# Kernel tuning notes

Hardware: AMD Instinct MI355X
Metric: run time of the kernel (lower is better)

Reference implementation:

```python
import jax, jax.numpy as jnp
import numpy as np

B, C, H, W = 4, 256, 64, 64
CH = C // 2  # inner channels


def setup_inputs() -> dict:
    key = jax.random.key(0)
    ks = jax.random.split(key, 9)
    s_in = 1.0 / np.sqrt(C)
    s_w = 1.0 / np.sqrt(CH)
    return {
        "x": jax.random.normal(ks[0], (B, C, H, W), dtype=jnp.float32),
        "theta_w": jax.random.normal(ks[1], (CH, C), dtype=jnp.float32) * s_in,
        "theta_b": jax.random.normal(ks[2], (CH,), dtype=jnp.float32) * s_in,
        "phi_w": jax.random.normal(ks[3], (CH, C), dtype=jnp.float32) * s_in,
        "phi_b": jax.random.normal(ks[4], (CH,), dtype=jnp.float32) * s_in,
        "g_w": jax.random.normal(ks[5], (CH, C), dtype=jnp.float32) * s_in,
        "g_b": jax.random.normal(ks[6], (CH,), dtype=jnp.float32) * s_in,
        "W_w": jax.random.normal(ks[7], (C, CH), dtype=jnp.float32) * s_w,
        "W_b": jax.random.normal(ks[8], (C,), dtype=jnp.float32) * s_w,
    }


def _proj(x_flat, w, b):
    # 1x1 conv == channel matmul; x_flat: [B, C, N] -> [B, O, N]
    return jnp.einsum("oc,bcn->bon", w, x_flat) + b[None, :, None]


def reference(x, theta_w, theta_b, phi_w, phi_b, g_w, g_b, W_w, W_b):
    b, c, h, w = x.shape
    n = h * w
    xf = x.reshape(b, c, n)
    theta = _proj(xf, theta_w, theta_b)  # [B, CH, N]
    phi = _proj(xf, phi_w, phi_b)        # [B, CH, N]
    g = _proj(xf, g_w, g_b)              # [B, CH, N]
    # scores[b,i,j] = theta[:, :, i] . phi[:, :, j]; softmax over j
    attn = jax.nn.softmax(jnp.einsum("bci,bcj->bij", theta, phi), axis=-1)
    # torch: bmm(g_x, attn) -> out[b,c,i] = sum_j g[b,c,j] * attn[b,j,i]
    out = jnp.einsum("bcj,bji->bci", g, attn)  # [B, CH, N]
    out = jnp.einsum("oc,bcn->bon", W_w, out) + W_b[None, :, None]
    return out.reshape(b, c, h, w) + x
```

## Files before the change

### kernel.cpp

```cpp
#include <hip/hip_runtime.h>
#include <hip/hip_bf16.h>
#include <math.h>

#define BB    4
#define CC    256
#define CHN   128
#define NN    4096

typedef short short8 __attribute__((ext_vector_type(8)));
typedef float f32x4  __attribute__((ext_vector_type(4)));
typedef unsigned short u16;
typedef u16  us4 __attribute__((ext_vector_type(4)));

#define MFMA16(a, b, c) __builtin_amdgcn_mfma_f32_16x16x32_bf16((a), (b), (c), 0, 0, 0)
#define LOG2E 1.4426950408889634f

#if __has_builtin(__builtin_amdgcn_exp2f)
#define EXP2F(x) __builtin_amdgcn_exp2f(x)
#else
#define EXP2F(x) exp2f(x)
#endif
#if __has_builtin(__builtin_amdgcn_logf)
#define LOG2F(x) __builtin_amdgcn_logf(x)
#else
#define LOG2F(x) log2f(x)
#endif

static __device__ __forceinline__ u16 f2bf(float f) {
    union { float f; unsigned u; } v; v.f = f;
    unsigned r = v.u + 0x7FFFu + ((v.u >> 16) & 1u);
    return (u16)(r >> 16);
}
static __device__ __forceinline__ unsigned pkbf(float a, float b) {
    __hip_bfloat162 h = __float22bfloat162_rn(make_float2(a, b));
    return *reinterpret_cast<unsigned*>(&h);
}
static __device__ __forceinline__ int sw128(int row, int u) {
    return row * 128 + ((u ^ (row & 7)) << 3);
}

__global__ __launch_bounds__(256) void k_cvtw(
    const float* __restrict__ tw, const float* __restrict__ pw,
    const float* __restrict__ gw, const float* __restrict__ Ww,
    u16* __restrict__ wall)
{
    int idx = (blockIdx.x * 256 + threadIdx.x) * 4;
    const float* s = (idx < 32768) ? tw
                   : (idx < 65536) ? pw
                   : (idx < 98304) ? gw : Ww;
    float sc = (idx < 32768) ? LOG2E : 1.0f;
    float4 v = *(const float4*)(s + (idx & 32767));
    us4 r = { f2bf(v.x * sc), f2bf(v.y * sc), f2bf(v.z * sc), f2bf(v.w * sc) };
    *(us4*)(wall + idx) = r;
}

__global__ __launch_bounds__(512) void k_proj(
    const float* __restrict__ x, const u16* __restrict__ wall,
    const float* __restrict__ tb, const float* __restrict__ pb,
    const float* __restrict__ gbias,
    u16* __restrict__ tht, u16* __restrict__ pht, u16* __restrict__ gg)
{
    __shared__ u16 xs[64 * 264];
    __shared__ u16 gbuf[128 * 68];
    const int tid = threadIdx.x;
    const int n0  = blockIdx.x * 64;
    const int b   = blockIdx.y;
    const int ln  = tid & 15, q = (tid >> 4) & 3, wid = tid >> 6;
    const int ow  = wid & 1, nw = wid >> 1;

    for (int p = 0; p < 8; ++p) {
        int id = p * 512 + tid;
        int c = id >> 4, n4 = (id & 15) * 4;
        float4 xv = *(const float4*)(x + ((size_t)b * CC + c) * NN + n0 + n4);
        xs[(n4 + 0) * 264 + c] = f2bf(xv.x);
        xs[(n4 + 1) * 264 + c] = f2bf(xv.y);
        xs[(n4 + 2) * 264 + c] = f2bf(xv.z);
        xs[(n4 + 3) * 264 + c] = f2bf(xv.w);
    }
    __syncthreads();

    short8 bfr[8];
    #pragma unroll
    for (int ks = 0; ks < 8; ++ks)
        bfr[ks] = *(const short8*)(&xs[(nw * 16 + ln) * 264 + ks * 32 + q * 8]);

    for (int pr = 0; pr < 3; ++pr) {
        const u16* wsrc = wall + pr * 32768;
        f32x4 acc[4];
        #pragma unroll
        for (int oo = 0; oo < 4; ++oo) acc[oo] = (f32x4){0.f, 0.f, 0.f, 0.f};
        for (int ks = 0; ks < 8; ++ks) {
            short8 a[4];
            #pragma unroll
            for (int oo = 0; oo < 4; ++oo)
                a[oo] = *(const short8*)(wsrc + (size_t)(ow*64 + oo*16 + ln) * 256 + ks*32 + q*8);
            #pragma unroll
            for (int oo = 0; oo < 4; ++oo)
                acc[oo] = MFMA16(a[oo], bfr[ks], acc[oo]);
        }
        const float* bias = (pr == 0) ? tb : (pr == 1 ? pb : gbias);
        const float bsc = (pr == 0) ? LOG2E : 1.0f;
        if (pr < 2) {
            u16* dst = (pr == 0) ? tht : pht;
            const int n = n0 + nw * 16 + ln;
            #pragma unroll
            for (int oo = 0; oo < 4; ++oo) {
                int o = ow * 64 + oo * 16 + q * 4;
                float4 bv = *(const float4*)(bias + o);
                f32x4 v = acc[oo];
                uint2 r = { pkbf(v.x + bv.x * bsc, v.y + bv.y * bsc),
                            pkbf(v.z + bv.z * bsc, v.w + bv.w * bsc) };
                *(uint2*)(dst + ((size_t)b * NN + n) * CHN + o) = r;
            }
        } else {
            const int nl = nw * 16 + ln;
            #pragma unroll
            for (int oo = 0; oo < 4; ++oo) {
                int o = ow * 64 + oo * 16 + q * 4;
                float4 bv = *(const float4*)(bias + o);
                f32x4 v = acc[oo];
                gbuf[(o + 0) * 68 + nl] = f2bf(v.x + bv.x);
                gbuf[(o + 1) * 68 + nl] = f2bf(v.y + bv.y);
                gbuf[(o + 2) * 68 + nl] = f2bf(v.z + bv.z);
                gbuf[(o + 3) * 68 + nl] = f2bf(v.w + bv.w);
            }
            __syncthreads();
            for (int p = 0; p < 4; ++p) {
                int id = p * 512 + tid;
                int c = id >> 4, n4 = (id & 15) * 4;
                us4 r = *(const us4*)(&gbuf[c * 68 + n4]);
                *(us4*)(gg + ((size_t)b * CHN + c) * NN + n0 + n4) = r;
            }
        }
    }
}

__global__ __launch_bounds__(512) void k_rowsum(
    const u16* __restrict__ tht, const u16* __restrict__ pht,
    float* __restrict__ Z)
{
    __shared__ u16 th_s[128 * 128];
    __shared__ u16 ph_s[128 * 128];
    __shared__ float zs[128][2];
    const int tid = threadIdx.x;
    const int j0  = blockIdx.x * 128;
    const int ih  = blockIdx.y;
    const int b   = blockIdx.z;
    const int ln  = tid & 15, q = (tid >> 4) & 3, wid = tid >> 6;
    const int jw  = wid & 3, iw = wid >> 2;

    {
        const u16* src = tht + ((size_t)b * NN + j0) * CHN;
        for (int p = 0; p < 4; ++p) {
            int id = p * 512 + tid;
            int row = id >> 4, u = id & 15;
            short8 v = *(const short8*)(src + row * 128 + u * 8);
            *(short8*)(&th_s[sw128(row, u)]) = v;
        }
    }
    __syncthreads();
    short8 ar[2][4];
    #pragma unroll
    for (int jj = 0; jj < 2; ++jj)
        #pragma unroll
        for (int ks = 0; ks < 4; ++ks)
            ar[jj][ks] = *(const short8*)(&th_s[sw128(jw*32 + jj*16 + ln, ks*4 + q)]);

    float zp[2][4];
    #pragma unroll
    for (int jj = 0; jj < 2; ++jj)
        #pragma unroll
        for (int r = 0; r < 4; ++r) zp[jj][r] = 0.f;

    const u16* phb = pht + ((size_t)b * NN + ih * 2048) * CHN;
    for (int is = 0; is < 16; ++is) {
        __syncthreads();
        for (int p = 0; p < 4; ++p) {
            int id = p * 512 + tid;
            int row = id >> 4, u = id & 15;
            short8 v = *(const short8*)(phb + (size_t)(is * 128 + row) * CHN + u * 8);
            *(short8*)(&ph_s[sw128(row, u)]) = v;
        }
        __syncthreads();

        f32x4 s[2][4];
        #pragma unroll
        for (int jj = 0; jj < 2; ++jj)
            #pragma unroll
            for (int ii = 0; ii < 4; ++ii) s[jj][ii] = (f32x4){0.f, 0.f, 0.f, 0.f};
        for (int ks = 0; ks < 4; ++ks) {
            short8 bb[4];
            #pragma unroll
            for (int ii = 0; ii < 4; ++ii)
                bb[ii] = *(const short8*)(&ph_s[sw128(iw*64 + ii*16 + ln, ks*4 + q)]);
            #pragma unroll
            for (int jj = 0; jj < 2; ++jj)
                #pragma unroll
                for (int ii = 0; ii < 4; ++ii)
                    s[jj][ii] = MFMA16(ar[jj][ks], bb[ii], s[jj][ii]);
        }
        #pragma unroll
        for (int jj = 0; jj < 2; ++jj)
            #pragma unroll
            for (int ii = 0; ii < 4; ++ii) {
                f32x4 v = s[jj][ii];
                zp[jj][0] += EXP2F(v.x);
                zp[jj][1] += EXP2F(v.y);
                zp[jj][2] += EXP2F(v.z);
                zp[jj][3] += EXP2F(v.w);
            }
    }

    #pragma unroll
    for (int jj = 0; jj < 2; ++jj)
        #pragma unroll
        for (int r = 0; r < 4; ++r) {
            float v = zp[jj][r];
            v += __shfl_xor(v, 1);
            v += __shfl_xor(v, 2);
            v += __shfl_xor(v, 4);
            v += __shfl_xor(v, 8);
            if (ln == 0) zs[jw*32 + jj*16 + q*4 + r][iw] = v;
        }
    __syncthreads();
    if (tid < 128)
        atomicAdd(&Z[(size_t)b * NN + j0 + tid], zs[tid][0] + zs[tid][1]);
}

__global__ __launch_bounds__(512, 2) void k_attn(
    const u16* __restrict__ tht, const u16* __restrict__ pht,
    const u16* __restrict__ gg, const float* __restrict__ Z,
    u16* __restrict__ innerT)
{
    __shared__ u16 th_s[128 * 128];
    __shared__ u16 g_s [128 * 128];
    __shared__ u16 E_s [256 * 128];
    const int tid = threadIdx.x;
    const int i0  = blockIdx.x * 256;
    const int jq  = blockIdx.y;
    const int b   = blockIdx.z;
    const int ln  = tid & 15, q = (tid >> 4) & 3, wid = tid >> 6;
    const int h1  = wid & 1;
    const int h2  = wid >> 1;

    const u16*  thb = tht + (size_t)b * NN * CHN;
    const u16*  ggb = gg  + (size_t)b * CHN * NN;
    const float* Zb = Z   + (size_t)b * NN;

    {
        const u16* src = pht + ((size_t)b * NN + i0) * CHN;
        for (int p = 0; p < 8; ++p) {
            int id = p * 512 + tid;
            int row = id >> 4, u = id & 15;
            short8 v = *(const short8*)(src + row * 128 + u * 8);
            *(short8*)(&E_s[sw128(row, u)]) = v;
        }
    }
    __syncthreads();
    short8 phr[4][4];
    #pragma unroll
    for (int ii = 0; ii < 4; ++ii)
        #pragma unroll
        for (int ks = 0; ks < 4; ++ks)
            phr[ii][ks] = *(const short8*)(&E_s[sw128(h2*64 + ii*16 + ln, ks*4 + q)]);

    f32x4 pacc[4][4];
    #pragma unroll
    for (int cc = 0; cc < 4; ++cc)
        #pragma unroll
        for (int ii = 0; ii < 4; ++ii) pacc[cc][ii] = (f32x4){0.f, 0.f, 0.f, 0.f};

    for (int js = 0; js < 8; ++js) {
        const int j0 = jq * 1024 + js * 128;
        __syncthreads();
        for (int p = 0; p < 4; ++p) {
            int id = p * 512 + tid;
            int row = id >> 4, u = id & 15;
            short8 v = *(const short8*)(thb + (size_t)(j0 + row) * CHN + u * 8);
            *(short8*)(&th_s[sw128(row, u)]) = v;
        }
        for (int p = 0; p < 4; ++p) {
            int id = p * 512 + tid;
            int row = id >> 4, u = id & 15;
            short8 v = *(const short8*)(ggb + (size_t)row * NN + j0 + u * 8);
            *(short8*)(&g_s[sw128(row, u)]) = v;
        }
        __syncthreads();

        #pragma unroll
        for (int jj = 0; jj < 4; ++jj) {
            const int jl = h1*64 + jj*16 + q*4;
            float4 Zv = *(const float4*)(Zb + j0 + jl);
            f32x4 cinit = { -LOG2F(Zv.x), -LOG2F(Zv.y), -LOG2F(Zv.z), -LOG2F(Zv.w) };
            f32x4 s0 = cinit, s1 = cinit, s2 = cinit, s3 = cinit;
            #pragma unroll
            for (int ks = 0; ks < 4; ++ks) {
                short8 a = *(const short8*)(&th_s[sw128(h1*64 + jj*16 + ln, ks*4 + q)]);
                s0 = MFMA16(a, phr[0][ks], s0);
                s1 = MFMA16(a, phr[1][ks], s1);
                s2 = MFMA16(a, phr[2][ks], s2);
                s3 = MFMA16(a, phr[3][ks], s3);
            }
            const int u = jl >> 3, off = jl & 7;
            f32x4 sv[4] = { s0, s1, s2, s3 };
            #pragma unroll
            for (int ii = 0; ii < 4; ++ii) {
                int ri = h2*64 + ii*16 + ln;
                f32x4 v = sv[ii];
                uint2 e = { pkbf(EXP2F(v.x), EXP2F(v.y)),
                            pkbf(EXP2F(v.z), EXP2F(v.w)) };
                *(uint2*)(&E_s[ri*128 + ((u ^ (ri & 7)) << 3) + off]) = e;
            }
        }
        __syncthreads();

        #pragma unroll
        for (int ks = 0; ks < 4; ++ks) {
            short8 be[4];
            #pragma unroll
            for (int ii = 0; ii < 4; ++ii)
                be[ii] = *(const short8*)(&E_s[sw128(h2*64 + ii*16 + ln, ks*4 + q)]);
            #pragma unroll
            for (int cc = 0; cc < 4; ++cc) {
                short8 ag = *(const short8*)(&g_s[sw128(h1*64 + cc*16 + ln, ks*4 + q)]);
                pacc[cc][0] = MFMA16(ag, be[0], pacc[cc][0]);
                pacc[cc][1] = MFMA16(ag, be[1], pacc[cc][1]);
                pacc[cc][2] = MFMA16(ag, be[2], pacc[cc][2]);
                pacc[cc][3] = MFMA16(ag, be[3], pacc[cc][3]);
            }
        }
    }

    u16* dst = innerT + ((size_t)jq * BB + b) * (size_t)NN * CHN;
    #pragma unroll
    for (int cc = 0; cc < 4; ++cc)
        #pragma unroll
        for (int ii = 0; ii < 4; ++ii) {
            int i = i0 + h2*64 + ii*16 + ln;
            int c = h1*64 + cc*16 + q*4;
            f32x4 v = pacc[cc][ii];
            uint2 r = { pkbf(v.x, v.y), pkbf(v.z, v.w) };
            *(uint2*)(dst + (size_t)i * CHN + c) = r;
        }
}

__global__ __launch_bounds__(512) void k_final(
    const u16* __restrict__ innerT, const float* __restrict__ x,
    const u16* __restrict__ Wwbf, const float* __restrict__ Wb,
    float* __restrict__ out)
{
    const int tid = threadIdx.x;
    const int n0  = blockIdx.x * 64;
    const int b   = blockIdx.y;
    const int ln  = tid & 15, q = (tid >> 4) & 3, wid = tid >> 6;

    f32x4 acc[4][2];
    #pragma unroll
    for (int nn = 0; nn < 4; ++nn)
        #pragma unroll
        for (int oo = 0; oo < 2; ++oo) acc[nn][oo] = (f32x4){0.f, 0.f, 0.f, 0.f};

    for (int jq = 0; jq < 4; ++jq) {
        const u16* src = innerT + ((size_t)jq * BB + b) * (size_t)NN * CHN;
        for (int ks = 0; ks < 4; ++ks) {
            short8 a[4], bw[2];
            #pragma unroll
            for (int nn = 0; nn < 4; ++nn)
                a[nn] = *(const short8*)(src + (size_t)(n0 + nn*16 + ln) * CHN + ks*32 + q*8);
            #pragma unroll
            for (int oo = 0; oo < 2; ++oo)
                bw[oo] = *(const short8*)(Wwbf + (size_t)(wid*32 + oo*16 + ln) * CHN + ks*32 + q*8);
            #pragma unroll
            for (int nn = 0; nn < 4; ++nn)
                #pragma unroll
                for (int oo = 0; oo < 2; ++oo)
                    acc[nn][oo] = MFMA16(a[nn], bw[oo], acc[nn][oo]);
        }
    }
    #pragma unroll
    for (int nn = 0; nn < 4; ++nn)
        #pragma unroll
        for (int oo = 0; oo < 2; ++oo) {
            int o = wid*32 + oo*16 + ln;
            int n = n0 + nn*16 + q*4;
            size_t idx = ((size_t)b * CC + o) * NN + n;
            float4 xv = *(const float4*)(x + idx);
            float wb = Wb[o];
            f32x4 v = acc[nn][oo];
            f32x4 r = { v.x + wb + xv.x, v.y + wb + xv.y,
                        v.z + wb + xv.z, v.w + wb + xv.w };
            *(f32x4*)(out + idx) = r;
        }
}

extern "C" void kernel_launch(void* const* d_in, const int* in_sizes, int n_in,
                              void* d_out, int out_size, void* d_ws, size_t ws_size,
                              hipStream_t stream)
{
    const float* x  = (const float*)d_in[0];
    const float* tw = (const float*)d_in[1];
    const float* tb = (const float*)d_in[2];
    const float* pw = (const float*)d_in[3];
    const float* pb = (const float*)d_in[4];
    const float* gw = (const float*)d_in[5];
    const float* gb = (const float*)d_in[6];
    const float* Ww = (const float*)d_in[7];
    const float* Wb = (const float*)d_in[8];
    float* out = (float*)d_out;

    char* p = (char*)d_ws;
    const size_t proj_u16 = (size_t)BB * NN * CHN;
    u16*   tht    = (u16*)p;   p += proj_u16 * 2;
    u16*   pht    = (u16*)p;   p += proj_u16 * 2;
    u16*   gg     = (u16*)p;   p += proj_u16 * 2;
    u16*   wall   = (u16*)p;   p += (size_t)131072 * 2;
    float* Z      = (float*)p; p += (size_t)BB * NN * 4;
    u16*   innerT = (u16*)p;

    hipMemsetAsync(Z, 0, (size_t)BB * NN * sizeof(float), stream);
    k_cvtw  <<<128, 256, 0, stream>>>(tw, pw, gw, Ww, wall);
    k_proj  <<<dim3(64, BB), 512, 0, stream>>>(x, wall, tb, pb, gb, tht, pht, gg);
    k_rowsum<<<dim3(32, 2, BB), 512, 0, stream>>>(tht, pht, Z);
    k_attn  <<<dim3(16, 4, BB), 512, 0, stream>>>(tht, pht, gg, Z, innerT);
    k_final <<<dim3(64, BB), 512, 0, stream>>>(innerT, x, wall + 98304, Wb, out);
}
```

Before: 205.3 us.

## Retile rowsum and attention kernels into smaller 256-thread blocks with larger grids

The rowsum kernel moves to 256-thread blocks that each cover a 512-wide slice of i, double-buffers the phi tiles in shared memory, and loads theta fragments straight from global into registers. Per-wave partial sums now go to Z with atomics instead of a shared-memory reduction. The attention kernel is retiled to 64-row i tiles with 64-wide j steps, uses a 64-column swizzle for g and E, and drops the 2-blocks-per-CU launch bound. Both grids grow fourfold, aiming for better CU occupancy and latency hiding. The cost is less reuse per block: theta and g are reloaded for every 64-row i tile, and there are more atomic operations on Z.

```diff
diff --git a/kernel.cpp b/kernel.cpp
--- a/kernel.cpp
+++ b/kernel.cpp
@@ -38,6 +38,9 @@
 static __device__ __forceinline__ int sw128(int row, int u) {
     return row * 128 + ((u ^ (row & 7)) << 3);
 }
+static __device__ __forceinline__ int sw64(int row, int u) {
+    return row * 64 + ((u ^ (row & 7)) << 3);
+}
 
 __global__ __launch_bounds__(256) void k_cvtw(
     const float* __restrict__ tw, const float* __restrict__ pw,
@@ -135,74 +138,73 @@
     }
 }
 
-__global__ __launch_bounds__(512) void k_rowsum(
+__global__ __launch_bounds__(256) void k_rowsum(
     const u16* __restrict__ tht, const u16* __restrict__ pht,
     float* __restrict__ Z)
 {
-    __shared__ u16 th_s[128 * 128];
-    __shared__ u16 ph_s[128 * 128];
-    __shared__ float zs[128][2];
+    __shared__ u16 ph_s[2][64 * 128];
     const int tid = threadIdx.x;
     const int j0  = blockIdx.x * 128;
-    const int ih  = blockIdx.y;
+    const int i00 = blockIdx.y * 512;
     const int b   = blockIdx.z;
     const int ln  = tid & 15, q = (tid >> 4) & 3, wid = tid >> 6;
-    const int jw  = wid & 3, iw = wid >> 2;
-
-    {
-        const u16* src = tht + ((size_t)b * NN + j0) * CHN;
-        for (int p = 0; p < 4; ++p) {
-            int id = p * 512 + tid;
-            int row = id >> 4, u = id & 15;
-            short8 v = *(const short8*)(src + row * 128 + u * 8);
-            *(short8*)(&th_s[sw128(row, u)]) = v;
-        }
-    }
-    __syncthreads();
-    short8 ar[2][4];
-    #pragma unroll
-    for (int jj = 0; jj < 2; ++jj)
+    const int jw  = wid & 1, iw = wid >> 1;
+    const u16* thb = tht + (size_t)b * NN * CHN;
+    const u16* phb = pht + (size_t)b * NN * CHN;
+
+    short8 ar[4][4];
+    #pragma unroll
+    for (int jj = 0; jj < 4; ++jj)
         #pragma unroll
         for (int ks = 0; ks < 4; ++ks)
-            ar[jj][ks] = *(const short8*)(&th_s[sw128(jw*32 + jj*16 + ln, ks*4 + q)]);
-
-    float zp[2][4];
-    #pragma unroll
-    for (int jj = 0; jj < 2; ++jj)
+            ar[jj][ks] = *(const short8*)(thb + (size_t)(j0 + jw*64 + jj*16 + ln) * CHN + ks*32 + q*8);
+
+    for (int p = 0; p < 4; ++p) {
+        int id = p * 256 + tid;
+        int row = id >> 4, u = id & 15;
+        short8 v = *(const short8*)(phb + (size_t)(i00 + row) * CHN + u * 8);
+        *(short8*)(&ph_s[0][sw128(row, u)]) = v;
+    }
+
+    float zp[4][4];
+    #pragma unroll
+    for (int jj = 0; jj < 4; ++jj)
         #pragma unroll
         for (int r = 0; r < 4; ++r) zp[jj][r] = 0.f;
 
-    const u16* phb = pht + ((size_t)b * NN + ih * 2048) * CHN;
-    for (int is = 0; is < 16; ++is) {
+    for (int is = 0; is < 8; ++is) {
         __syncthreads();
-        for (int p = 0; p < 4; ++p) {
-            int id = p * 512 + tid;
-            int row = id >> 4, u = id & 15;
-            short8 v = *(const short8*)(phb + (size_t)(is * 128 + row) * CHN + u * 8);
-            *(short8*)(&ph_s[sw128(row, u)]) = v;
-        }
-        __syncthreads();
-
-        f32x4 s[2][4];
-        #pragma unroll
-        for (int jj = 0; jj < 2; ++jj)
-            #pragma unroll
-            for (int ii = 0; ii < 4; ++ii) s[jj][ii] = (f32x4){0.f, 0.f, 0.f, 0.f};
+        if (is < 7) {
+            for (int p = 0; p < 4; ++p) {
+                int id = p * 256 + tid;
+                int row = id >> 4, u = id & 15;
+                short8 v = *(const short8*)(phb + (size_t)(i00 + (is+1)*64 + row) * CHN + u * 8);
+                *(short8*)(&ph_s[(is + 1) & 1][sw128(row, u)]) = v;
+            }
+        }
+        const u16* cur = ph_s[is & 1];
+
+        f32x4 s[4][2];
+        #pragma unroll
+        for (int jj = 0; jj < 4; ++jj)
+            #pragma unroll
+            for (int ii = 0; ii < 2; ++ii) s[jj][ii] = (f32x4){0.f, 0.f, 0.f, 0.f};
+        #pragma unroll
         for (int ks = 0; ks < 4; ++ks) {
-            short8 bb[4];
-            #pragma unroll
-            for (int ii = 0; ii < 4; ++ii)
-                bb[ii] = *(const short8*)(&ph_s[sw128(iw*64 + ii*16 + ln, ks*4 + q)]);
-            #pragma unroll
-            for (int jj = 0; jj < 2; ++jj)
-                #pragma unroll
-                for (int ii = 0; ii < 4; ++ii)
-                    s[jj][ii] = MFMA16(ar[jj][ks], bb[ii], s[jj][ii]);
-        }
-        #pragma unroll
-        for (int jj = 0; jj < 2; ++jj)
-            #pragma unroll
-            for (int ii = 0; ii < 4; ++ii) {
+            short8 bb[2];
+            #pragma unroll
+            for (int ii = 0; ii < 2; ++ii)
+                bb[ii] = *(const short8*)(&cur[sw128(iw*32 + ii*16 + ln, ks*4 + q)]);
+            #pragma unroll
+            for (int jj = 0; jj < 4; ++jj) {
+                s[jj][0] = MFMA16(ar[jj][ks], bb[0], s[jj][0]);
+                s[jj][1] = MFMA16(ar[jj][ks], bb[1], s[jj][1]);
+            }
+        }
+        #pragma unroll
+        for (int jj = 0; jj < 4; ++jj)
+            #pragma unroll
+            for (int ii = 0; ii < 2; ++ii) {
                 f32x4 v = s[jj][ii];
                 zp[jj][0] += EXP2F(v.x);
                 zp[jj][1] += EXP2F(v.y);
@@ -212,7 +214,7 @@
     }
 
     #pragma unroll
-    for (int jj = 0; jj < 2; ++jj)
+    for (int jj = 0; jj < 4; ++jj)
         #pragma unroll
         for (int r = 0; r < 4; ++r) {
             float v = zp[jj][r];
@@ -220,82 +222,67 @@
             v += __shfl_xor(v, 2);
             v += __shfl_xor(v, 4);
             v += __shfl_xor(v, 8);
-            if (ln == 0) zs[jw*32 + jj*16 + q*4 + r][iw] = v;
-        }
-    __syncthreads();
-    if (tid < 128)
-        atomicAdd(&Z[(size_t)b * NN + j0 + tid], zs[tid][0] + zs[tid][1]);
-}
-
-__global__ __launch_bounds__(512, 2) void k_attn(
+            if (ln == 0)
+                atomicAdd(&Z[(size_t)b * NN + j0 + jw*64 + jj*16 + q*4 + r], v);
+        }
+}
+
+__global__ __launch_bounds__(256) void k_attn(
     const u16* __restrict__ tht, const u16* __restrict__ pht,
     const u16* __restrict__ gg, const float* __restrict__ Z,
     u16* __restrict__ innerT)
 {
-    __shared__ u16 th_s[128 * 128];
-    __shared__ u16 g_s [128 * 128];
-    __shared__ u16 E_s [256 * 128];
+    __shared__ u16 th_s[64 * 128];
+    __shared__ u16 g_s [128 * 64];
+    __shared__ u16 E_s [64 * 64];
     const int tid = threadIdx.x;
-    const int i0  = blockIdx.x * 256;
+    const int i0  = blockIdx.x * 64;
     const int jq  = blockIdx.y;
     const int b   = blockIdx.z;
     const int ln  = tid & 15, q = (tid >> 4) & 3, wid = tid >> 6;
-    const int h1  = wid & 1;
-    const int h2  = wid >> 1;
 
     const u16*  thb = tht + (size_t)b * NN * CHN;
     const u16*  ggb = gg  + (size_t)b * CHN * NN;
     const float* Zb = Z   + (size_t)b * NN;
 
-    {
-        const u16* src = pht + ((size_t)b * NN + i0) * CHN;
-        for (int p = 0; p < 8; ++p) {
-            int id = p * 512 + tid;
-            int row = id >> 4, u = id & 15;
-            short8 v = *(const short8*)(src + row * 128 + u * 8);
-            *(short8*)(&E_s[sw128(row, u)]) = v;
-        }
-    }
-    __syncthreads();
     short8 phr[4][4];
     #pragma unroll
     for (int ii = 0; ii < 4; ++ii)
         #pragma unroll
         for (int ks = 0; ks < 4; ++ks)
-            phr[ii][ks] = *(const short8*)(&E_s[sw128(h2*64 + ii*16 + ln, ks*4 + q)]);
-
-    f32x4 pacc[4][4];
-    #pragma unroll
-    for (int cc = 0; cc < 4; ++cc)
+            phr[ii][ks] = *(const short8*)(pht + ((size_t)b * NN + i0 + ii*16 + ln) * CHN + ks*32 + q*8);
+
+    f32x4 pacc[2][4];
+    #pragma unroll
+    for (int cc = 0; cc < 2; ++cc)
         #pragma unroll
         for (int ii = 0; ii < 4; ++ii) pacc[cc][ii] = (f32x4){0.f, 0.f, 0.f, 0.f};
 
-    for (int js = 0; js < 8; ++js) {
-        const int j0 = jq * 1024 + js * 128;
+    for (int js = 0; js < 16; ++js) {
+        const int j0 = jq * 1024 + js * 64;
         __syncthreads();
         for (int p = 0; p < 4; ++p) {
-            int id = p * 512 + tid;
+            int id = p * 256 + tid;
             int row = id >> 4, u = id & 15;
             short8 v = *(const short8*)(thb + (size_t)(j0 + row) * CHN + u * 8);
             *(short8*)(&th_s[sw128(row, u)]) = v;
         }
         for (int p = 0; p < 4; ++p) {
-            int id = p * 512 + tid;
-            int row = id >> 4, u = id & 15;
+            int id = p * 256 + tid;
+            int row = id >> 3, u = id & 7;
             short8 v = *(const short8*)(ggb + (size_t)row * NN + j0 + u * 8);
-            *(short8*)(&g_s[sw128(row, u)]) = v;
+            *(short8*)(&g_s[sw64(row, u)]) = v;
         }
         __syncthreads();
 
-        #pragma unroll
-        for (int jj = 0; jj < 4; ++jj) {
-            const int jl = h1*64 + jj*16 + q*4;
+        {
+            const int jl = wid * 16 + q * 4;
             float4 Zv = *(const float4*)(Zb + j0 + jl);
             f32x4 cinit = { -LOG2F(Zv.x), -LOG2F(Zv.y), -LOG2F(Zv.z), -LOG2F(Zv.w) };
             f32x4 s0 = cinit, s1 = cinit, s2 = cinit, s3 = cinit;
             #pragma unroll
             for (int ks = 0; ks < 4; ++ks) {
-                short8 a = *(const short8*)(&th_s[sw128(h1*64 + jj*16 + ln, ks*4 + q)]);
+                short8 a = *(const short8*)(&th_s[sw128(wid*16 + ln, ks*4 + q)]);
                 s0 = MFMA16(a, phr[0][ks], s0);
                 s1 = MFMA16(a, phr[1][ks], s1);
                 s2 = MFMA16(a, phr[2][ks], s2);
@@ -305,24 +292,24 @@
             f32x4 sv[4] = { s0, s1, s2, s3 };
             #pragma unroll
             for (int ii = 0; ii < 4; ++ii) {
-                int ri = h2*64 + ii*16 + ln;
+                int ri = ii*16 + ln;
                 f32x4 v = sv[ii];
                 uint2 e = { pkbf(EXP2F(v.x), EXP2F(v.y)),
                             pkbf(EXP2F(v.z), EXP2F(v.w)) };
-                *(uint2*)(&E_s[ri*128 + ((u ^ (ri & 7)) << 3) + off]) = e;
+                *(uint2*)(&E_s[ri*64 + ((u ^ (ri & 7)) << 3) + off]) = e;
             }
         }
         __syncthreads();
 
         #pragma unroll
-        for (int ks = 0; ks < 4; ++ks) {
+        for (int ks = 0; ks < 2; ++ks) {
             short8 be[4];
             #pragma unroll
             for (int ii = 0; ii < 4; ++ii)
-                be[ii] = *(const short8*)(&E_s[sw128(h2*64 + ii*16 + ln, ks*4 + q)]);
-            #pragma unroll
-            for (int cc = 0; cc < 4; ++cc) {
-                short8 ag = *(const short8*)(&g_s[sw128(h1*64 + cc*16 + ln, ks*4 + q)]);
+                be[ii] = *(const short8*)(&E_s[sw64(ii*16 + ln, ks*4 + q)]);
+            #pragma unroll
+            for (int cc = 0; cc < 2; ++cc) {
+                short8 ag = *(const short8*)(&g_s[sw64(wid*32 + cc*16 + ln, ks*4 + q)]);
                 pacc[cc][0] = MFMA16(ag, be[0], pacc[cc][0]);
                 pacc[cc][1] = MFMA16(ag, be[1], pacc[cc][1]);
                 pacc[cc][2] = MFMA16(ag, be[2], pacc[cc][2]);
@@ -333,11 +320,11 @@
 
     u16* dst = innerT + ((size_t)jq * BB + b) * (size_t)NN * CHN;
     #pragma unroll
-    for (int cc = 0; cc < 4; ++cc)
+    for (int cc = 0; cc < 2; ++cc)
         #pragma unroll
         for (int ii = 0; ii < 4; ++ii) {
-            int i = i0 + h2*64 + ii*16 + ln;
-            int c = h1*64 + cc*16 + q*4;
+            int i = i0 + ii*16 + ln;
+            int c = wid*32 + cc*16 + q*4;
             f32x4 v = pacc[cc][ii];
             uint2 r = { pkbf(v.x, v.y), pkbf(v.z, v.w) };
             *(uint2*)(dst + (size_t)i * CHN + c) = r;
@@ -420,7 +407,7 @@
     hipMemsetAsync(Z, 0, (size_t)BB * NN * sizeof(float), stream);
     k_cvtw  <<<128, 256, 0, stream>>>(tw, pw, gw, Ww, wall);
     k_proj  <<<dim3(64, BB), 512, 0, stream>>>(x, wall, tb, pb, gb, tht, pht, gg);
-    k_rowsum<<<dim3(32, 2, BB), 512, 0, stream>>>(tht, pht, Z);
-    k_attn  <<<dim3(16, 4, BB), 512, 0, stream>>>(tht, pht, gg, Z, innerT);
+    k_rowsum<<<dim3(32, 8, BB), 256, 0, stream>>>(tht, pht, Z);
+    k_attn  <<<dim3(64, 4, BB), 256, 0, stream>>>(tht, pht, gg, Z, innerT);
     k_final <<<dim3(64, BB), 512, 0, stream>>>(innerT, x, wall + 98304, Wb, out);
 }
```

Measured after the change: 245.4 us. +19.5%, slower.
